# Performance work log

Measured on AMD Instinct MI355X. Metric: run time of the kernel, lower is better.

Reference implementation:

```python
import jax, jax.numpy as jnp
import numpy as np

N, K, D = 131072, 2048, 512


def setup_inputs() -> dict:
    key = jax.random.key(0)
    kx, kc = jax.random.split(key)
    x = jax.random.normal(kx, (N, D), dtype=jnp.float32)
    cluster_centers = jax.random.normal(kc, (K, D), dtype=jnp.float32)
    return {"x": x, "cluster_centers": cluster_centers}


def reference(x, cluster_centers):
    # d_{nk} = ||x_n - c_k||_2; argmin over k.
    x2 = jnp.sum(x * x, axis=-1, keepdims=True)            # [N,1]
    c2 = jnp.sum(cluster_centers * cluster_centers, -1)    # [K]
    d2 = x2 + c2 - 2.0 * (x @ cluster_centers.T)           # [N,K]
    # sqrt is monotonic, so argmin over squared distances equals argmin over L2 norms
    return jnp.argmin(d2, axis=-1)                          # [N] int
```

## Files before the change

### kernel.cpp

```cpp
#include <hip/hip_runtime.h>


#define N_PTS 131072
#define K_CL  2048
#define D_DIM 512
#define BM 128
#define BN 128
#define BK 32

typedef _Float16 half8  __attribute__((ext_vector_type(8)));
typedef _Float16 half4v __attribute__((ext_vector_type(4)));
typedef float    floatx4 __attribute__((ext_vector_type(4)));

#define GLL(g, l) __builtin_amdgcn_global_load_lds( \
    (__attribute__((address_space(1))) void*)(g),   \
    (__attribute__((address_space(3))) void*)(l), 16, 0, 0)

__global__ void row_norms_kernel(const float* __restrict__ A,
                                 float* __restrict__ out, int rows) {
    int gid  = blockIdx.x * blockDim.x + threadIdx.x;
    int wave = gid >> 6;
    int lane = gid & 63;
    if (wave >= rows) return;
    const float4* a = (const float4*)(A + (size_t)wave * D_DIM);
    float4 p = a[lane];
    float4 q = a[lane + 64];
    float s = p.x*p.x + p.y*p.y + p.z*p.z + p.w*p.w
            + q.x*q.x + q.y*q.y + q.z*q.z + q.w*q.w;
    #pragma unroll
    for (int off = 32; off > 0; off >>= 1) s += __shfl_down(s, off, 64);
    if (lane == 0) out[wave] = s;
}

__global__ void conv_f16x2_kernel(const float* __restrict__ src,
                                  _Float16* __restrict__ hi,
                                  _Float16* __restrict__ lo, int n4) {
    int i = blockIdx.x * blockDim.x + threadIdx.x;
    if (i >= n4) return;
    float4 v = ((const float4*)src)[i];
    half4v h, l;
    h.x = (_Float16)v.x; h.y = (_Float16)v.y;
    h.z = (_Float16)v.z; h.w = (_Float16)v.w;
    l.x = (_Float16)(v.x - (float)h.x);
    l.y = (_Float16)(v.y - (float)h.y);
    l.z = (_Float16)(v.z - (float)h.z);
    l.w = (_Float16)(v.w - (float)h.w);
    *(half4v*)(hi + (size_t)i * 4) = h;
    *(half4v*)(lo + (size_t)i * 4) = l;
}

template<bool XPRE, bool CPRE>
__global__ __launch_bounds__(256, 3)
void kmeans_mfma(const float* __restrict__ X, const float* __restrict__ C,
                 const _Float16* __restrict__ Xhi, const _Float16* __restrict__ Xlo,
                 const _Float16* __restrict__ Chi, const _Float16* __restrict__ Clo,
                 const float* __restrict__ c2g, int* __restrict__ out) {
    __shared__ __align__(16) _Float16 sXh[BM * BK], sXl[BM * BK];
    __shared__ __align__(16) _Float16 sCh[BN * BK], sCl[BN * BK];
    __shared__ float c2s[K_CL];
    __shared__ float x2s[BM];

    const int tid  = threadIdx.x;
    const int lane = tid & 63;
    const int w    = tid >> 6;
    const int wti  = w >> 1;
    const int wtj  = w & 1;
    const int q    = lane >> 4;
    const int m16  = lane & 15;
    const int rowBase = blockIdx.x * BM;

    if (CPRE) {
        for (int i = tid; i < K_CL / 4; i += 256)
            ((float4*)c2s)[i] = ((const float4*)c2g)[i];
    } else {
        for (int k = tid; k < K_CL; k += 256) {
            const float4* cp = (const float4*)(C + (size_t)k * D_DIM);
            float s0 = 0.f, s1 = 0.f;
            for (int j = 0; j < D_DIM / 4; j += 2) {
                float4 a = cp[j], b = cp[j + 1];
                s0 += a.x*a.x + a.y*a.y + a.z*a.z + a.w*a.w;
                s1 += b.x*b.x + b.y*b.y + b.z*b.z + b.w*b.w;
            }
            c2s[k] = s0 + s1;
        }
    }
    {
        int r = tid & 127, h = tid >> 7;
        const float4* xp = (const float4*)(X + (size_t)(rowBase + r) * D_DIM + h * 256);
        float s0 = 0.f, s1 = 0.f;
        for (int j = 0; j < 64; j += 2) {
            float4 a = xp[j], b = xp[j + 1];
            s0 += a.x*a.x + a.y*a.y + a.z*a.z + a.w*a.w;
            s1 += b.x*b.x + b.y*b.y + b.z*b.z + b.w*b.w;
        }
        ((float*)sXh)[tid] = s0 + s1;
    }
    __syncthreads();
    if (tid < BM) x2s[tid] = ((float*)sXh)[tid] + ((float*)sXh)[tid + 128];

    float bestV[4][4];
    int   bestI[4][4];
    #pragma unroll
    for (int ti = 0; ti < 4; ++ti)
        #pragma unroll
        for (int r = 0; r < 4; ++r) { bestV[ti][r] = 3.4e38f; bestI[ti][r] = 0; }

    const int s_c4 = tid & 7;
    const int s_r0 = tid >> 3;

    #pragma unroll 1
    for (int kt = 0; kt < K_CL / BN; ++kt) {
        const int k0 = kt * BN;
        floatx4 acc[4][4];
        #pragma unroll
        for (int ti = 0; ti < 4; ++ti)
            #pragma unroll
            for (int tj = 0; tj < 4; ++tj) acc[ti][tj] = (floatx4){0.f, 0.f, 0.f, 0.f};

        #pragma unroll 1
        for (int dt = 0; dt < D_DIM / BK; ++dt) {
            const int d0 = dt * BK;
            __syncthreads();
            if (XPRE) {
                #pragma unroll
                for (int s = 0; s < 2; ++s) {
                    int c = w * 2 + s;
                    int r = c * 16 + (lane >> 2);
                    size_t go = (size_t)(rowBase + r) * D_DIM + d0 + (lane & 3) * 8;
                    GLL(Xhi + go, &sXh[c * 512]);
                    GLL(Xlo + go, &sXl[c * 512]);
                }
            } else {
                #pragma unroll
                for (int p = 0; p < 4; ++p) {
                    int r = s_r0 + p * 32;
                    float4 v = *(const float4*)&X[(size_t)(rowBase + r) * D_DIM + d0 + s_c4 * 4];
                    half4v h, l;
                    h.x = (_Float16)v.x; h.y = (_Float16)v.y;
                    h.z = (_Float16)v.z; h.w = (_Float16)v.w;
                    l.x = (_Float16)(v.x - (float)h.x);
                    l.y = (_Float16)(v.y - (float)h.y);
                    l.z = (_Float16)(v.z - (float)h.z);
                    l.w = (_Float16)(v.w - (float)h.w);
                    *(half4v*)&sXh[r * BK + s_c4 * 4] = h;
                    *(half4v*)&sXl[r * BK + s_c4 * 4] = l;
                }
            }
            if (CPRE) {
                #pragma unroll
                for (int s = 0; s < 2; ++s) {
                    int c = w * 2 + s;
                    int r = c * 16 + (lane >> 2);
                    size_t go = (size_t)(k0 + r) * D_DIM + d0 + (lane & 3) * 8;
                    GLL(Chi + go, &sCh[c * 512]);
                    GLL(Clo + go, &sCl[c * 512]);
                }
            } else {
                #pragma unroll
                for (int p = 0; p < 4; ++p) {
                    int r = s_r0 + p * 32;
                    float4 v = *(const float4*)&C[(size_t)(k0 + r) * D_DIM + d0 + s_c4 * 4];
                    half4v h, l;
                    h.x = (_Float16)v.x; h.y = (_Float16)v.y;
                    h.z = (_Float16)v.z; h.w = (_Float16)v.w;
                    l.x = (_Float16)(v.x - (float)h.x);
                    l.y = (_Float16)(v.y - (float)h.y);
                    l.z = (_Float16)(v.z - (float)h.z);
                    l.w = (_Float16)(v.w - (float)h.w);
                    *(half4v*)&sCh[r * BK + s_c4 * 4] = h;
                    *(half4v*)&sCl[r * BK + s_c4 * 4] = l;
                }
            }
            __syncthreads();

            half8 ah[4], al[4];
            #pragma unroll
            for (int ti = 0; ti < 4; ++ti) {
                int row = wti * 64 + ti * 16 + m16;
                ah[ti] = *(const half8*)&sXh[row * BK + q * 8];
                al[ti] = *(const half8*)&sXl[row * BK + q * 8];
            }
            #pragma unroll
            for (int tj = 0; tj < 4; ++tj) {
                int col = wtj * 64 + tj * 16 + m16;
                half8 bh = *(const half8*)&sCh[col * BK + q * 8];
                half8 bl = *(const half8*)&sCl[col * BK + q * 8];
                #pragma unroll
                for (int ti = 0; ti < 4; ++ti) {
                    floatx4 a = acc[ti][tj];
                    a = __builtin_amdgcn_mfma_f32_16x16x32_f16(ah[ti], bh, a, 0, 0, 0);
                    a = __builtin_amdgcn_mfma_f32_16x16x32_f16(ah[ti], bl, a, 0, 0, 0);
                    a = __builtin_amdgcn_mfma_f32_16x16x32_f16(al[ti], bh, a, 0, 0, 0);
                    acc[ti][tj] = a;
                }
            }
        }

        #pragma unroll
        for (int tj = 0; tj < 4; ++tj) {
            int col = k0 + wtj * 64 + tj * 16 + m16;
            float cv = c2s[col];
            #pragma unroll
            for (int ti = 0; ti < 4; ++ti)
                #pragma unroll
                for (int r = 0; r < 4; ++r) {
                    float s = x2s[wti * 64 + ti * 16 + q * 4 + r] + cv;
                    float v = s - 2.0f * acc[ti][tj][r];
                    if (v < bestV[ti][r]) { bestV[ti][r] = v; bestI[ti][r] = col; }
                }
        }
    }

    #pragma unroll
    for (int ti = 0; ti < 4; ++ti)
        #pragma unroll
        for (int r = 0; r < 4; ++r) {
            float v = bestV[ti][r]; int ix = bestI[ti][r];
            #pragma unroll
            for (int off = 1; off < 16; off <<= 1) {
                float ov = __shfl_xor(v, off, 64);
                int   oi = __shfl_xor(ix, off, 64);
                if (ov < v || (ov == v && oi < ix)) { v = ov; ix = oi; }
            }
            bestV[ti][r] = v; bestI[ti][r] = ix;
        }

    __syncthreads();
    float* rv  = (float*)sXh;
    int*   rix = (int*)sCh;
    if (m16 == 0) {
        #pragma unroll
        for (int ti = 0; ti < 4; ++ti)
            #pragma unroll
            for (int r = 0; r < 4; ++r) {
                int rloc = wti * 64 + ti * 16 + q * 4 + r;
                rv[rloc * 2 + wtj]  = bestV[ti][r];
                rix[rloc * 2 + wtj] = bestI[ti][r];
            }
    }
    __syncthreads();
    if (tid < BM) {
        float v0 = rv[tid * 2], v1 = rv[tid * 2 + 1];
        int   i0 = rix[tid * 2], i1 = rix[tid * 2 + 1];
        out[rowBase + tid] = (v1 < v0 || (v1 == v0 && i1 < i0)) ? i1 : i0;
    }
}

extern "C" void kernel_launch(void* const* d_in, const int* in_sizes, int n_in,
                              void* d_out, int out_size, void* d_ws, size_t ws_size,
                              hipStream_t stream) {
    const float* X = (const float*)d_in[0];
    const float* C = (const float*)d_in[1];
    int* out = (int*)d_out;

    char* ws = (char*)d_ws;
    const size_t c2_off  = 0;
    const size_t chi_off = (size_t)K_CL * 4;
    const size_t clo_off = chi_off + (size_t)K_CL * D_DIM * 2;
    const size_t xhi_off = clo_off + (size_t)K_CL * D_DIM * 2;
    const size_t xlo_off = xhi_off + (size_t)N_PTS * D_DIM * 2;
    const size_t need_C    = xhi_off;
    const size_t need_full = xlo_off + (size_t)N_PTS * D_DIM * 2;

    if (ws_size >= need_full) {
        float*    c2  = (float*)(ws + c2_off);
        _Float16* Chi = (_Float16*)(ws + chi_off);
        _Float16* Clo = (_Float16*)(ws + clo_off);
        _Float16* Xhi = (_Float16*)(ws + xhi_off);
        _Float16* Xlo = (_Float16*)(ws + xlo_off);
        row_norms_kernel<<<(K_CL * 64) / 256, 256, 0, stream>>>(C, c2, K_CL);
        conv_f16x2_kernel<<<(K_CL * D_DIM / 4) / 256, 256, 0, stream>>>(
            C, Chi, Clo, K_CL * D_DIM / 4);
        conv_f16x2_kernel<<<(N_PTS * D_DIM / 4 + 255) / 256, 256, 0, stream>>>(
            X, Xhi, Xlo, N_PTS * D_DIM / 4);
        kmeans_mfma<true, true><<<N_PTS / BM, 256, 0, stream>>>(
            X, C, Xhi, Xlo, Chi, Clo, c2, out);
    } else if (ws_size >= need_C) {
        float*    c2  = (float*)(ws + c2_off);
        _Float16* Chi = (_Float16*)(ws + chi_off);
        _Float16* Clo = (_Float16*)(ws + clo_off);
        row_norms_kernel<<<(K_CL * 64) / 256, 256, 0, stream>>>(C, c2, K_CL);
        conv_f16x2_kernel<<<(K_CL * D_DIM / 4) / 256, 256, 0, stream>>>(
            C, Chi, Clo, K_CL * D_DIM / 4);
        kmeans_mfma<false, true><<<N_PTS / BM, 256, 0, stream>>>(
            X, C, nullptr, nullptr, Chi, Clo, c2, out);
    } else {
        kmeans_mfma<false, false><<<N_PTS / BM, 256, 0, stream>>>(
            X, C, nullptr, nullptr, nullptr, nullptr, nullptr, out);
    }
}
```

Measured before the change: 1.348 ms.

## Register-prefetch next tile and pad LDS rows in flattened MFMA loop

Replaces direct global-to-LDS loads with register prefetch of the next tile, issued after the barrier so the global loads overlap the MFMA work on the current tile. The K and D loops are flattened into one loop, and the argmin epilogue runs every 16 iterations, resetting the accumulators. LDS rows are padded from 32 to 40 halves to reduce bank conflicts on the half8 fragment reads. This adds register pressure from the prefetch buffers under a 3-blocks-per-CU launch bound, and removes the C-only precompute path.

```diff
diff --git a/kernel.cpp b/kernel.cpp
--- a/kernel.cpp
+++ b/kernel.cpp
@@ -7,14 +7,12 @@
 #define BM 128
 #define BN 128
 #define BK 32
+#define LDK 40
+#define NIT ((K_CL / BN) * (D_DIM / BK))
 
 typedef _Float16 half8  __attribute__((ext_vector_type(8)));
 typedef _Float16 half4v __attribute__((ext_vector_type(4)));
 typedef float    floatx4 __attribute__((ext_vector_type(4)));
-
-#define GLL(g, l) __builtin_amdgcn_global_load_lds( \
-    (__attribute__((address_space(1))) void*)(g),   \
-    (__attribute__((address_space(3))) void*)(l), 16, 0, 0)
 
 __global__ void row_norms_kernel(const float* __restrict__ A,
                                  float* __restrict__ out, int rows) {
@@ -34,29 +32,34 @@
 
 __global__ void conv_f16x2_kernel(const float* __restrict__ src,
                                   _Float16* __restrict__ hi,
-                                  _Float16* __restrict__ lo, int n4) {
-    int i = blockIdx.x * blockDim.x + threadIdx.x;
-    if (i >= n4) return;
-    float4 v = ((const float4*)src)[i];
-    half4v h, l;
-    h.x = (_Float16)v.x; h.y = (_Float16)v.y;
-    h.z = (_Float16)v.z; h.w = (_Float16)v.w;
-    l.x = (_Float16)(v.x - (float)h.x);
-    l.y = (_Float16)(v.y - (float)h.y);
-    l.z = (_Float16)(v.z - (float)h.z);
-    l.w = (_Float16)(v.w - (float)h.w);
-    *(half4v*)(hi + (size_t)i * 4) = h;
-    *(half4v*)(lo + (size_t)i * 4) = l;
-}
-
-template<bool XPRE, bool CPRE>
+                                  _Float16* __restrict__ lo, int rows) {
+    int gid = blockIdx.x * blockDim.x + threadIdx.x;
+    int row = gid >> 6, lane = gid & 63;
+    if (row >= rows) return;
+    const float4* a = (const float4*)(src + (size_t)row * D_DIM);
+    float4 p = a[lane];
+    float4 q = a[lane + 64];
+    half4v ph, pl, qh, ql;
+    ph.x=(_Float16)p.x; ph.y=(_Float16)p.y; ph.z=(_Float16)p.z; ph.w=(_Float16)p.w;
+    qh.x=(_Float16)q.x; qh.y=(_Float16)q.y; qh.z=(_Float16)q.z; qh.w=(_Float16)q.w;
+    pl.x=(_Float16)(p.x-(float)ph.x); pl.y=(_Float16)(p.y-(float)ph.y);
+    pl.z=(_Float16)(p.z-(float)ph.z); pl.w=(_Float16)(p.w-(float)ph.w);
+    ql.x=(_Float16)(q.x-(float)qh.x); ql.y=(_Float16)(q.y-(float)qh.y);
+    ql.z=(_Float16)(q.z-(float)qh.z); ql.w=(_Float16)(q.w-(float)qh.w);
+    *(half4v*)(hi + (size_t)row * D_DIM +       lane * 4) = ph;
+    *(half4v*)(hi + (size_t)row * D_DIM + 256 + lane * 4) = qh;
+    *(half4v*)(lo + (size_t)row * D_DIM +       lane * 4) = pl;
+    *(half4v*)(lo + (size_t)row * D_DIM + 256 + lane * 4) = ql;
+}
+
+template<bool PRE>
 __global__ __launch_bounds__(256, 3)
 void kmeans_mfma(const float* __restrict__ X, const float* __restrict__ C,
                  const _Float16* __restrict__ Xhi, const _Float16* __restrict__ Xlo,
                  const _Float16* __restrict__ Chi, const _Float16* __restrict__ Clo,
                  const float* __restrict__ c2g, int* __restrict__ out) {
-    __shared__ __align__(16) _Float16 sXh[BM * BK], sXl[BM * BK];
-    __shared__ __align__(16) _Float16 sCh[BN * BK], sCl[BN * BK];
+    __shared__ __align__(16) _Float16 sXh[BM * LDK], sXl[BM * LDK];
+    __shared__ __align__(16) _Float16 sCh[BN * LDK], sCl[BN * LDK];
     __shared__ float c2s[K_CL];
     __shared__ float x2s[BM];
 
@@ -69,7 +72,8 @@
     const int m16  = lane & 15;
     const int rowBase = blockIdx.x * BM;
 
-    if (CPRE) {
+    if (PRE) {
+        #pragma unroll
         for (int i = tid; i < K_CL / 4; i += 256)
             ((float4*)c2s)[i] = ((const float4*)c2g)[i];
     } else {
@@ -105,109 +109,113 @@
         #pragma unroll
         for (int r = 0; r < 4; ++r) { bestV[ti][r] = 3.4e38f; bestI[ti][r] = 0; }
 
-    const int s_c4 = tid & 7;
-    const int s_r0 = tid >> 3;
+    const int s_row = tid >> 2;
+    const int s_f4  = tid & 3;
+
+    float4 rXh[2], rXl[2], rCh[2], rCl[2];
+
+    auto prefetch = [&](int nit) {
+        const int nkt = nit >> 4, ndt = nit & 15;
+        const int d0 = ndt * BK + s_f4 * 8;
+        #pragma unroll
+        for (int u = 0; u < 2; ++u) {
+            size_t xr = (size_t)(rowBase + s_row + u * 64) * D_DIM + d0;
+            size_t cr = (size_t)(nkt * BN + s_row + u * 64) * D_DIM + d0;
+            if (PRE) {
+                rXh[u] = *(const float4*)(Xhi + xr);
+                rXl[u] = *(const float4*)(Xlo + xr);
+                rCh[u] = *(const float4*)(Chi + cr);
+                rCl[u] = *(const float4*)(Clo + cr);
+            } else {
+                rXh[u] = *(const float4*)(X + xr);
+                rXl[u] = *(const float4*)(X + xr + 4);
+                rCh[u] = *(const float4*)(C + cr);
+                rCl[u] = *(const float4*)(C + cr + 4);
+            }
+        }
+    };
+
+    auto store_tiles = [&]() {
+        #pragma unroll
+        for (int u = 0; u < 2; ++u) {
+            int r = s_row + u * 64;
+            if (PRE) {
+                *(float4*)&sXh[r * LDK + s_f4 * 8] = rXh[u];
+                *(float4*)&sXl[r * LDK + s_f4 * 8] = rXl[u];
+                *(float4*)&sCh[r * LDK + s_f4 * 8] = rCh[u];
+                *(float4*)&sCl[r * LDK + s_f4 * 8] = rCl[u];
+            } else {
+                float fx[8] = {rXh[u].x, rXh[u].y, rXh[u].z, rXh[u].w,
+                               rXl[u].x, rXl[u].y, rXl[u].z, rXl[u].w};
+                float fc[8] = {rCh[u].x, rCh[u].y, rCh[u].z, rCh[u].w,
+                               rCl[u].x, rCl[u].y, rCl[u].z, rCl[u].w};
+                half8 xh, xl, ch, cl;
+                #pragma unroll
+                for (int j = 0; j < 8; ++j) {
+                    xh[j] = (_Float16)fx[j]; xl[j] = (_Float16)(fx[j] - (float)xh[j]);
+                    ch[j] = (_Float16)fc[j]; cl[j] = (_Float16)(fc[j] - (float)ch[j]);
+                }
+                *(half8*)&sXh[r * LDK + s_f4 * 8] = xh;
+                *(half8*)&sXl[r * LDK + s_f4 * 8] = xl;
+                *(half8*)&sCh[r * LDK + s_f4 * 8] = ch;
+                *(half8*)&sCl[r * LDK + s_f4 * 8] = cl;
+            }
+        }
+    };
+
+    floatx4 acc[4][4];
+    #pragma unroll
+    for (int ti = 0; ti < 4; ++ti)
+        #pragma unroll
+        for (int tj = 0; tj < 4; ++tj) acc[ti][tj] = (floatx4){0.f, 0.f, 0.f, 0.f};
+
+    prefetch(0);
 
     #pragma unroll 1
-    for (int kt = 0; kt < K_CL / BN; ++kt) {
-        const int k0 = kt * BN;
-        floatx4 acc[4][4];
-        #pragma unroll
-        for (int ti = 0; ti < 4; ++ti)
-            #pragma unroll
-            for (int tj = 0; tj < 4; ++tj) acc[ti][tj] = (floatx4){0.f, 0.f, 0.f, 0.f};
-
-        #pragma unroll 1
-        for (int dt = 0; dt < D_DIM / BK; ++dt) {
-            const int d0 = dt * BK;
-            __syncthreads();
-            if (XPRE) {
+    for (int it = 0; it < NIT; ++it) {
+        __syncthreads();
+        store_tiles();
+        __syncthreads();
+        if (it + 1 < NIT) prefetch(it + 1);
+
+        half8 ah[4], al[4];
+        #pragma unroll
+        for (int ti = 0; ti < 4; ++ti) {
+            int row = wti * 64 + ti * 16 + m16;
+            ah[ti] = *(const half8*)&sXh[row * LDK + q * 8];
+            al[ti] = *(const half8*)&sXl[row * LDK + q * 8];
+        }
+        #pragma unroll
+        for (int tj = 0; tj < 4; ++tj) {
+            int col = wtj * 64 + tj * 16 + m16;
+            half8 bh = *(const half8*)&sCh[col * LDK + q * 8];
+            half8 bl = *(const half8*)&sCl[col * LDK + q * 8];
+            #pragma unroll
+            for (int ti = 0; ti < 4; ++ti) {
+                floatx4 a = acc[ti][tj];
+                a = __builtin_amdgcn_mfma_f32_16x16x32_f16(ah[ti], bh, a, 0, 0, 0);
+                a = __builtin_amdgcn_mfma_f32_16x16x32_f16(ah[ti], bl, a, 0, 0, 0);
+                a = __builtin_amdgcn_mfma_f32_16x16x32_f16(al[ti], bh, a, 0, 0, 0);
+                acc[ti][tj] = a;
+            }
+        }
+
+        if ((it & 15) == 15) {
+            const int k0 = (it >> 4) * BN;
+            #pragma unroll
+            for (int tj = 0; tj < 4; ++tj) {
+                int col = k0 + wtj * 64 + tj * 16 + m16;
+                float cv = c2s[col];
                 #pragma unroll
-                for (int s = 0; s < 2; ++s) {
-                    int c = w * 2 + s;
-                    int r = c * 16 + (lane >> 2);
-                    size_t go = (size_t)(rowBase + r) * D_DIM + d0 + (lane & 3) * 8;
-                    GLL(Xhi + go, &sXh[c * 512]);
-                    GLL(Xlo + go, &sXl[c * 512]);
-                }
-            } else {
-                #pragma unroll
-                for (int p = 0; p < 4; ++p) {
-                    int r = s_r0 + p * 32;
-                    float4 v = *(const float4*)&X[(size_t)(rowBase + r) * D_DIM + d0 + s_c4 * 4];
-                    half4v h, l;
-                    h.x = (_Float16)v.x; h.y = (_Float16)v.y;
-                    h.z = (_Float16)v.z; h.w = (_Float16)v.w;
-                    l.x = (_Float16)(v.x - (float)h.x);
-                    l.y = (_Float16)(v.y - (float)h.y);
-                    l.z = (_Float16)(v.z - (float)h.z);
-                    l.w = (_Float16)(v.w - (float)h.w);
-                    *(half4v*)&sXh[r * BK + s_c4 * 4] = h;
-                    *(half4v*)&sXl[r * BK + s_c4 * 4] = l;
-                }
-            }
-            if (CPRE) {
-                #pragma unroll
-                for (int s = 0; s < 2; ++s) {
-                    int c = w * 2 + s;
-                    int r = c * 16 + (lane >> 2);
-                    size_t go = (size_t)(k0 + r) * D_DIM + d0 + (lane & 3) * 8;
-                    GLL(Chi + go, &sCh[c * 512]);
-                    GLL(Clo + go, &sCl[c * 512]);
-                }
-            } else {
-                #pragma unroll
-                for (int p = 0; p < 4; ++p) {
-                    int r = s_r0 + p * 32;
-                    float4 v = *(const float4*)&C[(size_t)(k0 + r) * D_DIM + d0 + s_c4 * 4];
-                    half4v h, l;
-                    h.x = (_Float16)v.x; h.y = (_Float16)v.y;
-                    h.z = (_Float16)v.z; h.w = (_Float16)v.w;
-                    l.x = (_Float16)(v.x - (float)h.x);
-                    l.y = (_Float16)(v.y - (float)h.y);
-                    l.z = (_Float16)(v.z - (float)h.z);
-                    l.w = (_Float16)(v.w - (float)h.w);
-                    *(half4v*)&sCh[r * BK + s_c4 * 4] = h;
-                    *(half4v*)&sCl[r * BK + s_c4 * 4] = l;
-                }
-            }
-            __syncthreads();
-
-            half8 ah[4], al[4];
-            #pragma unroll
-            for (int ti = 0; ti < 4; ++ti) {
-                int row = wti * 64 + ti * 16 + m16;
-                ah[ti] = *(const half8*)&sXh[row * BK + q * 8];
-                al[ti] = *(const half8*)&sXl[row * BK + q * 8];
-            }
-            #pragma unroll
-            for (int tj = 0; tj < 4; ++tj) {
-                int col = wtj * 64 + tj * 16 + m16;
-                half8 bh = *(const half8*)&sCh[col * BK + q * 8];
-                half8 bl = *(const half8*)&sCl[col * BK + q * 8];
-                #pragma unroll
-                for (int ti = 0; ti < 4; ++ti) {
-                    floatx4 a = acc[ti][tj];
-                    a = __builtin_amdgcn_mfma_f32_16x16x32_f16(ah[ti], bh, a, 0, 0, 0);
-                    a = __builtin_amdgcn_mfma_f32_16x16x32_f16(ah[ti], bl, a, 0, 0, 0);
-                    a = __builtin_amdgcn_mfma_f32_16x16x32_f16(al[ti], bh, a, 0, 0, 0);
-                    acc[ti][tj] = a;
-                }
-            }
-        }
-
-        #pragma unroll
-        for (int tj = 0; tj < 4; ++tj) {
-            int col = k0 + wtj * 64 + tj * 16 + m16;
-            float cv = c2s[col];
-            #pragma unroll
-            for (int ti = 0; ti < 4; ++ti)
-                #pragma unroll
-                for (int r = 0; r < 4; ++r) {
-                    float s = x2s[wti * 64 + ti * 16 + q * 4 + r] + cv;
-                    float v = s - 2.0f * acc[ti][tj][r];
-                    if (v < bestV[ti][r]) { bestV[ti][r] = v; bestI[ti][r] = col; }
-                }
+                for (int ti = 0; ti < 4; ++ti)
+                    #pragma unroll
+                    for (int r = 0; r < 4; ++r) {
+                        float s = x2s[wti * 64 + ti * 16 + q * 4 + r] + cv;
+                        float v = s - 2.0f * acc[ti][tj][r];
+                        if (v < bestV[ti][r]) { bestV[ti][r] = v; bestI[ti][r] = col; }
+                        acc[ti][tj][r] = 0.0f;
+                    }
+            }
         }
     }
 
@@ -259,7 +267,6 @@
     const size_t clo_off = chi_off + (size_t)K_CL * D_DIM * 2;
     const size_t xhi_off = clo_off + (size_t)K_CL * D_DIM * 2;
     const size_t xlo_off = xhi_off + (size_t)N_PTS * D_DIM * 2;
-    const size_t need_C    = xhi_off;
     const size_t need_full = xlo_off + (size_t)N_PTS * D_DIM * 2;
 
     if (ws_size >= need_full) {
@@ -269,23 +276,12 @@
         _Float16* Xhi = (_Float16*)(ws + xhi_off);
         _Float16* Xlo = (_Float16*)(ws + xlo_off);
         row_norms_kernel<<<(K_CL * 64) / 256, 256, 0, stream>>>(C, c2, K_CL);
-        conv_f16x2_kernel<<<(K_CL * D_DIM / 4) / 256, 256, 0, stream>>>(
-            C, Chi, Clo, K_CL * D_DIM / 4);
-        conv_f16x2_kernel<<<(N_PTS * D_DIM / 4 + 255) / 256, 256, 0, stream>>>(
-            X, Xhi, Xlo, N_PTS * D_DIM / 4);
-        kmeans_mfma<true, true><<<N_PTS / BM, 256, 0, stream>>>(
+        conv_f16x2_kernel<<<(K_CL * 64) / 256, 256, 0, stream>>>(C, Chi, Clo, K_CL);
+        conv_f16x2_kernel<<<(N_PTS * 64) / 256, 256, 0, stream>>>(X, Xhi, Xlo, N_PTS);
+        kmeans_mfma<true><<<N_PTS / BM, 256, 0, stream>>>(
             X, C, Xhi, Xlo, Chi, Clo, c2, out);
-    } else if (ws_size >= need_C) {
-        float*    c2  = (float*)(ws + c2_off);
-        _Float16* Chi = (_Float16*)(ws + chi_off);
-        _Float16* Clo = (_Float16*)(ws + clo_off);
-        row_norms_kernel<<<(K_CL * 64) / 256, 256, 0, stream>>>(C, c2, K_CL);
-        conv_f16x2_kernel<<<(K_CL * D_DIM / 4) / 256, 256, 0, stream>>>(
-            C, Chi, Clo, K_CL * D_DIM / 4);
-        kmeans_mfma<false, true><<<N_PTS / BM, 256, 0, stream>>>(
-            X, C, nullptr, nullptr, Chi, Clo, c2, out);
     } else {
-        kmeans_mfma<false, false><<<N_PTS / BM, 256, 0, stream>>>(
+        kmeans_mfma<false><<<N_PTS / BM, 256, 0, stream>>>(
             X, C, nullptr, nullptr, nullptr, nullptr, nullptr, out);
     }
 }
```

Result: slower. 3.548 ms (+163.3%).
